# Performance work log

Hardware: AMD Instinct MI355X
Metric: run time of the kernel (lower is better)

The kernel has to match this reference:

```python
import jax, jax.numpy as jnp
import numpy as np

N = 100000          # active sites
C_IN = 256          # inplanes == outplanes
C_MID = 64          # innerplanes
K = 9               # 3x3 kernel offsets (2D)


def setup_inputs() -> dict:
    key = jax.random.key(0)
    ks = jax.random.split(key, 12)
    features = jax.random.normal(ks[0], (N, C_IN), dtype=jnp.float32)
    # submanifold rulebook: for each active site, index of active neighbor per
    # kernel offset; sentinel N = no active neighbor, center (offset 4) = self
    idx = jax.random.randint(ks[1], (N, K), 0, N, dtype=jnp.int32)
    drop = jax.random.uniform(ks[2], (N, K)) < 0.3
    idx = jnp.where(drop, jnp.int32(N), idx)
    neighbor_idx = idx.at[:, 4].set(jnp.arange(N, dtype=jnp.int32))
    s = 0.05
    return {
        "features": features,
        "neighbor_idx": neighbor_idx,
        "w1": jax.random.normal(ks[3], (C_IN, C_MID), dtype=jnp.float32) * s,
        "scale1": jnp.ones((C_MID,), jnp.float32),
        "bias1": jnp.zeros((C_MID,), jnp.float32),
        "w2": jax.random.normal(ks[4], (K, C_MID, C_MID), dtype=jnp.float32) * s,
        "scale2": jnp.ones((C_MID,), jnp.float32),
        "bias2": jnp.zeros((C_MID,), jnp.float32),
        "w3": jax.random.normal(ks[5], (C_MID, C_IN), dtype=jnp.float32) * s,
        "scale3": jnp.ones((C_IN,), jnp.float32),
        "bias3": jnp.zeros((C_IN,), jnp.float32),
    }


def reference(features, neighbor_idx, w1, scale1, bias1, w2, scale2, bias2,
              w3, scale3, bias3):
    # conv1: 1x1 submanifold conv == per-site matmul; affine BN; ReLU
    out = jax.nn.relu(features @ w1 * scale1 + bias1)            # [N, C_MID]
    # conv2: 3x3 submanifold conv via rulebook gather-matmul-accumulate
    padded = jnp.concatenate([out, jnp.zeros((1, C_MID), out.dtype)], axis=0)
    gathered = padded[neighbor_idx]                               # [N, K, C_MID]
    out = jnp.einsum('nkc,kcd->nd', gathered, w2)                 # [N, C_MID]
    out = jax.nn.relu(out * scale2 + bias2)
    # conv3: 1x1 conv; affine BN; residual add (downsample=None); ReLU
    out = out @ w3 * scale3 + bias3 + features                    # [N, C_IN]
    return jax.nn.relu(out)
```

## Files before the change

### kernel.cpp

```cpp
#include <hip/hip_runtime.h>
#include <stdint.h>

#define C_IN 256
#define C_MID 64
#define KOFF 9

typedef __attribute__((ext_vector_type(8))) short bf16x8;
typedef __attribute__((ext_vector_type(4))) short short4v;
typedef __attribute__((ext_vector_type(4))) float f32x4;
typedef __attribute__((ext_vector_type(4))) float float4v;

__device__ inline unsigned short f2bf(float f) {
    union { float f; unsigned u; } x; x.f = f;
    unsigned r = x.u + 0x7FFFu + ((x.u >> 16) & 1u);
    return (unsigned short)(r >> 16);
}

__global__ void prep_kernel(const float* __restrict__ w1, const float* __restrict__ s1,
                            const float* __restrict__ w2, const float* __restrict__ s2,
                            const float* __restrict__ w3, const float* __restrict__ s3,
                            unsigned short* __restrict__ w1t,
                            unsigned short* __restrict__ w2t,
                            unsigned short* __restrict__ w3t,
                            unsigned short* __restrict__ zrow) {
    int tid = blockIdx.x * blockDim.x + threadIdx.x;
    int stride = gridDim.x * blockDim.x;
    for (int i = tid; i < C_MID * C_IN; i += stride) {
        int n = i / C_IN, k = i % C_IN;
        w1t[i] = f2bf(w1[k * C_MID + n] * s1[n]);
    }
    for (int i = tid; i < KOFF * C_MID * C_MID; i += stride) {
        int k = i / (C_MID * C_MID);
        int r = i % (C_MID * C_MID);
        int d = r / C_MID, c = r % C_MID;
        w2t[i] = f2bf(w2[(k * C_MID + c) * C_MID + d] * s2[d]);
    }
    for (int i = tid; i < C_IN * C_MID; i += stride) {
        int e = i / C_MID, c = i % C_MID;
        w3t[i] = f2bf(w3[c * C_IN + e] * s3[e]);
    }
    for (int i = tid; i < C_MID; i += stride) zrow[i] = 0;
}

__global__ __launch_bounds__(256, 4) void conv1_kernel(
    const float* __restrict__ feat, const unsigned short* __restrict__ w1t,
    const float* __restrict__ b1, unsigned short* __restrict__ out1,
    int N, int ntiles)
{
    __shared__ __align__(16) unsigned short sW1[16384];

    int t = threadIdx.x;
    int wave = t >> 6;
    int lane = t & 63;
    int l15 = lane & 15;
    int quad = lane >> 4;

    const bf16x8* w1c = reinterpret_cast<const bf16x8*>(w1t);
    bf16x8* sW1c = reinterpret_cast<bf16x8*>(sW1);
#pragma unroll
    for (int it = 0; it < 8; ++it) {
        int s = it * 256 + t;
        int l = s & 15, ct = (s >> 4) & 3, q = (s >> 6) & 3, kk = s >> 8;
        sW1c[s] = w1c[(ct * 16 + l) * 32 + kk * 4 + q];
    }
    __syncthreads();

    for (int tile = blockIdx.x; tile < ntiles; tile += gridDim.x) {
        int site = tile * 64 + wave * 16 + l15;
        int sitec = site < N ? site : (N - 1);

        float4v fr0[8];
#pragma unroll
        for (int kk = 0; kk < 4; ++kk) {
            const float4v* p = reinterpret_cast<const float4v*>(
                feat + (size_t)sitec * C_IN + kk * 32 + quad * 8);
            fr0[kk * 2] = p[0];
            fr0[kk * 2 + 1] = p[1];
        }
        __builtin_amdgcn_sched_barrier(0);

        float4v fr1[8];
#pragma unroll
        for (int kk = 0; kk < 4; ++kk) {
            const float4v* p = reinterpret_cast<const float4v*>(
                feat + (size_t)sitec * C_IN + (kk + 4) * 32 + quad * 8);
            fr1[kk * 2] = p[0];
            fr1[kk * 2 + 1] = p[1];
        }
        __builtin_amdgcn_sched_barrier(0);

        f32x4 acc[4] = {};
#pragma unroll
        for (int kk = 0; kk < 4; ++kk) {
            union { unsigned short s[8]; bf16x8 v; } ua;
#pragma unroll
            for (int j = 0; j < 4; ++j) {
                ua.s[j] = f2bf(fr0[kk * 2][j]);
                ua.s[4 + j] = f2bf(fr0[kk * 2 + 1][j]);
            }
#pragma unroll
            for (int ct = 0; ct < 4; ++ct) {
                bf16x8 fa = sW1c[((kk * 4 + quad) * 4 + ct) * 16 + l15];
                acc[ct] = __builtin_amdgcn_mfma_f32_16x16x32_bf16(fa, ua.v, acc[ct], 0, 0, 0);
            }
        }
#pragma unroll
        for (int kk = 0; kk < 4; ++kk) {
            union { unsigned short s[8]; bf16x8 v; } ua;
#pragma unroll
            for (int j = 0; j < 4; ++j) {
                ua.s[j] = f2bf(fr1[kk * 2][j]);
                ua.s[4 + j] = f2bf(fr1[kk * 2 + 1][j]);
            }
#pragma unroll
            for (int ct = 0; ct < 4; ++ct) {
                bf16x8 fa = sW1c[(((kk + 4) * 4 + quad) * 4 + ct) * 16 + l15];
                acc[ct] = __builtin_amdgcn_mfma_f32_16x16x32_bf16(fa, ua.v, acc[ct], 0, 0, 0);
            }
        }
        if (site < N) {
#pragma unroll
            for (int ct = 0; ct < 4; ++ct) {
                float4v bb = *reinterpret_cast<const float4v*>(b1 + ct * 16 + quad * 4);
                union { unsigned short s[4]; short4v v; } o;
#pragma unroll
                for (int reg = 0; reg < 4; ++reg)
                    o.s[reg] = f2bf(fmaxf(acc[ct][reg] + bb[reg], 0.f));
                *reinterpret_cast<short4v*>(out1 + (size_t)site * C_MID + ct * 16 + quad * 4) = o.v;
            }
        }
    }
}

__global__ __launch_bounds__(256, 2) void conv23_kernel(
    const float* __restrict__ feat, const int* __restrict__ nbr,
    const unsigned short* __restrict__ out1, const unsigned short* __restrict__ w2t,
    const float* __restrict__ b2, const unsigned short* __restrict__ w3t,
    const float* __restrict__ b3, float* __restrict__ out, int N)
{
    __shared__ __align__(16) unsigned short sWB[21504];
    __shared__ int sNbr[64 * KOFF];

    int t = threadIdx.x;
    int wave = t >> 6;
    int lane = t & 63;
    int l15 = lane & 15;
    int quad = lane >> 4;
    int rt = wave * 16 + l15;
    int site = blockIdx.x * 64 + rt;
    int sitec = site < N ? site : (N - 1);

    bf16x8* sWBc = reinterpret_cast<bf16x8*>(sWB);
    const bf16x8* w2c = reinterpret_cast<const bf16x8*>(w2t);

#pragma unroll
    for (int it = 0; it < 10; ++it) {
        int s = it * 256 + t;
        int l = s & 15, ct = (s >> 4) & 3, q = (s >> 6) & 3, kk = (s >> 8) & 1, k = s >> 9;
        sWBc[s] = w2c[k * 512 + (ct * 16 + l) * 8 + kk * 4 + q];
    }
#pragma unroll
    for (int i = 0; i < 3; ++i) {
        int j = i * 256 + t;
        if (j < 64 * KOFF) {
            int g = blockIdx.x * 64 * KOFF + j;
            sNbr[j] = (g < N * KOFF) ? nbr[g] : N;
        }
    }
    __syncthreads();

    int nb[KOFF];
#pragma unroll
    for (int k = 0; k < KOFF; ++k) nb[k] = sNbr[rt * KOFF + k];

    bf16x8 ga[KOFF][2];
#pragma unroll
    for (int k = 0; k < KOFF; ++k) {
        const bf16x8* pg = reinterpret_cast<const bf16x8*>(out1 + (size_t)nb[k] * C_MID + quad * 8);
        ga[k][0] = pg[0];
        ga[k][1] = pg[4];
    }
    __builtin_amdgcn_sched_barrier(0);

    f32x4 acc2[4] = {};
#pragma unroll
    for (int k = 0; k < 5; ++k) {
#pragma unroll
        for (int kk = 0; kk < 2; ++kk) {
#pragma unroll
            for (int ct = 0; ct < 4; ++ct) {
                bf16x8 fa = sWBc[((k * 2 + kk) * 4 + quad) * 64 + ct * 16 + l15];
                acc2[ct] = __builtin_amdgcn_mfma_f32_16x16x32_bf16(fa, ga[k][kk], acc2[ct], 0, 0, 0);
            }
        }
    }
    __syncthreads();

#pragma unroll
    for (int it = 0; it < 8; ++it) {
        int s = it * 256 + t;
        int l = s & 15, ct = (s >> 4) & 3, q = (s >> 6) & 3, kk = (s >> 8) & 1, k2 = s >> 9;
        sWBc[s] = w2c[(5 + k2) * 512 + (ct * 16 + l) * 8 + kk * 4 + q];
    }
    __syncthreads();
#pragma unroll
    for (int k = 5; k < KOFF; ++k) {
        int kloc = k - 5;
#pragma unroll
        for (int kk = 0; kk < 2; ++kk) {
#pragma unroll
            for (int ct = 0; ct < 4; ++ct) {
                bf16x8 fa = sWBc[((kloc * 2 + kk) * 4 + quad) * 64 + ct * 16 + l15];
                acc2[ct] = __builtin_amdgcn_mfma_f32_16x16x32_bf16(fa, ga[k][kk], acc2[ct], 0, 0, 0);
            }
        }
    }
    float4v rf[16];
#pragma unroll
    for (int c2 = 0; c2 < 16; ++c2)
        rf[c2] = __builtin_nontemporal_load(reinterpret_cast<const float4v*>(
            feat + (size_t)sitec * C_IN + c2 * 16 + quad * 4));
    __builtin_amdgcn_sched_barrier(0);
    __syncthreads();

    unsigned short* mid = &sWB[16384];
#pragma unroll
    for (int ct = 0; ct < 4; ++ct) {
        float4v bb = *reinterpret_cast<const float4v*>(b2 + ct * 16 + quad * 4);
        union { unsigned short s[4]; short4v v; } o;
#pragma unroll
        for (int reg = 0; reg < 4; ++reg)
            o.s[reg] = f2bf(fmaxf(acc2[ct][reg] + bb[reg], 0.f));
        *reinterpret_cast<short4v*>(&mid[rt * 72 + ct * 16 + quad * 4]) = o.v;
    }
    const bf16x8* w3c = reinterpret_cast<const bf16x8*>(w3t);
#pragma unroll
    for (int it = 0; it < 8; ++it) {
        int s = it * 256 + t;
        int l = s & 15, c2 = (s >> 4) & 15, q = (s >> 8) & 3, kk = (s >> 10) & 1;
        sWBc[s] = w3c[(c2 * 16 + l) * 8 + kk * 4 + q];
    }
    __syncthreads();

    f32x4 acc3[16] = {};
#pragma unroll
    for (int kk = 0; kk < 2; ++kk) {
        bf16x8 fb = *reinterpret_cast<const bf16x8*>(
            &mid[rt * 72 + kk * 32 + quad * 8]);
#pragma unroll
        for (int c2 = 0; c2 < 16; ++c2) {
            bf16x8 fa = sWBc[((kk * 4 + quad) * 16 + c2) * 16 + l15];
            acc3[c2] = __builtin_amdgcn_mfma_f32_16x16x32_bf16(fa, fb, acc3[c2], 0, 0, 0);
        }
    }
    if (site < N) {
#pragma unroll
        for (int c2 = 0; c2 < 16; ++c2) {
            float4v bb = *reinterpret_cast<const float4v*>(b3 + c2 * 16 + quad * 4);
            float4v o;
#pragma unroll
            for (int reg = 0; reg < 4; ++reg)
                o[reg] = fmaxf(acc3[c2][reg] + bb[reg] + rf[c2][reg], 0.f);
            __builtin_nontemporal_store(o, reinterpret_cast<float4v*>(
                out + (size_t)site * C_IN + c2 * 16 + quad * 4));
        }
    }
}

extern "C" void kernel_launch(void* const* d_in, const int* in_sizes, int n_in,
                              void* d_out, int out_size, void* d_ws, size_t ws_size,
                              hipStream_t stream) {
    const float* feat = (const float*)d_in[0];
    const int*   nbr  = (const int*)d_in[1];
    const float* w1   = (const float*)d_in[2];
    const float* s1   = (const float*)d_in[3];
    const float* b1   = (const float*)d_in[4];
    const float* w2   = (const float*)d_in[5];
    const float* s2   = (const float*)d_in[6];
    const float* b2   = (const float*)d_in[7];
    const float* w3   = (const float*)d_in[8];
    const float* s3   = (const float*)d_in[9];
    const float* b3   = (const float*)d_in[10];
    float* out = (float*)d_out;
    int N = in_sizes[0] / C_IN;

    char* ws = (char*)d_ws;
    unsigned short* w1t  = (unsigned short*)(ws);
    unsigned short* w2t  = (unsigned short*)(ws + 32768);
    unsigned short* w3t  = (unsigned short*)(ws + 32768 + 73728);
    unsigned short* out1 = (unsigned short*)(ws + 139264);

    prep_kernel<<<80, 256, 0, stream>>>(w1, s1, w2, s2, w3, s3, w1t, w2t, w3t,
                                        out1 + (size_t)N * C_MID);
    int ntiles = (N + 63) / 64;
    int nblk1 = ntiles < 1024 ? ntiles : 1024;
    conv1_kernel<<<nblk1, 256, 0, stream>>>(feat, w1t, b1, out1, N, ntiles);
    conv23_kernel<<<ntiles, 256, 0, stream>>>(feat, nbr, out1, w2t, b2, w3t, b3, out, N);
}
```

Before: 259.2 us.

## Make conv23 persistent with all weights resident in LDS and prefetched neighbors

```diff
diff --git a/kernel.cpp b/kernel.cpp
--- a/kernel.cpp
+++ b/kernel.cpp
@@ -132,14 +132,14 @@
     }
 }
 
-__global__ __launch_bounds__(256, 2) void conv23_kernel(
+__global__ __launch_bounds__(512, 2) void conv23_kernel(
     const float* __restrict__ feat, const int* __restrict__ nbr,
     const unsigned short* __restrict__ out1, const unsigned short* __restrict__ w2t,
     const float* __restrict__ b2, const unsigned short* __restrict__ w3t,
-    const float* __restrict__ b3, float* __restrict__ out, int N)
+    const float* __restrict__ b3, float* __restrict__ out, int N, int ntiles)
 {
-    __shared__ __align__(16) unsigned short sWB[21504];
-    __shared__ int sNbr[64 * KOFF];
+    __shared__ __align__(16) unsigned short sW[53248];
+    __shared__ __align__(16) unsigned short sMid[128 * 72];
 
     int t = threadIdx.x;
     int wave = t >> 6;
@@ -147,123 +147,120 @@
     int l15 = lane & 15;
     int quad = lane >> 4;
     int rt = wave * 16 + l15;
-    int site = blockIdx.x * 64 + rt;
-    int sitec = site < N ? site : (N - 1);
-
-    bf16x8* sWBc = reinterpret_cast<bf16x8*>(sWB);
+
+    bf16x8* sWc = reinterpret_cast<bf16x8*>(sW);
     const bf16x8* w2c = reinterpret_cast<const bf16x8*>(w2t);
-
-#pragma unroll
-    for (int it = 0; it < 10; ++it) {
-        int s = it * 256 + t;
+    const bf16x8* w3c = reinterpret_cast<const bf16x8*>(w3t);
+
+#pragma unroll
+    for (int it = 0; it < 9; ++it) {
+        int s = it * 512 + t;
         int l = s & 15, ct = (s >> 4) & 3, q = (s >> 6) & 3, kk = (s >> 8) & 1, k = s >> 9;
-        sWBc[s] = w2c[k * 512 + (ct * 16 + l) * 8 + kk * 4 + q];
-    }
-#pragma unroll
-    for (int i = 0; i < 3; ++i) {
-        int j = i * 256 + t;
-        if (j < 64 * KOFF) {
-            int g = blockIdx.x * 64 * KOFF + j;
-            sNbr[j] = (g < N * KOFF) ? nbr[g] : N;
-        }
+        sWc[s] = w2c[k * 512 + (ct * 16 + l) * 8 + kk * 4 + q];
+    }
+#pragma unroll
+    for (int it = 0; it < 4; ++it) {
+        int s = it * 512 + t;
+        int l = s & 15, c2 = (s >> 4) & 15, q = (s >> 8) & 3, kk = (s >> 10) & 1;
+        sWc[4608 + s] = w3c[(c2 * 16 + l) * 8 + kk * 4 + q];
     }
     __syncthreads();
 
     int nb[KOFF];
-#pragma unroll
-    for (int k = 0; k < KOFF; ++k) nb[k] = sNbr[rt * KOFF + k];
-
-    bf16x8 ga[KOFF][2];
-#pragma unroll
-    for (int k = 0; k < KOFF; ++k) {
-        const bf16x8* pg = reinterpret_cast<const bf16x8*>(out1 + (size_t)nb[k] * C_MID + quad * 8);
-        ga[k][0] = pg[0];
-        ga[k][1] = pg[4];
-    }
-    __builtin_amdgcn_sched_barrier(0);
-
-    f32x4 acc2[4] = {};
-#pragma unroll
-    for (int k = 0; k < 5; ++k) {
+    {
+        int site0 = blockIdx.x * 128 + rt;
+        bool v0 = site0 < N;
+        int base0 = v0 ? site0 * KOFF : 0;
+#pragma unroll
+        for (int k = 0; k < KOFF; ++k) {
+            int tmp = nbr[base0 + k];
+            nb[k] = v0 ? tmp : N;
+        }
+    }
+
+    for (int tile = blockIdx.x; tile < ntiles; tile += gridDim.x) {
+        int site = tile * 128 + rt;
+        int sitec = site < N ? site : (N - 1);
+
+        bf16x8 ga[KOFF][2];
+#pragma unroll
+        for (int k = 0; k < KOFF; ++k) {
+            const bf16x8* pg = reinterpret_cast<const bf16x8*>(
+                out1 + (size_t)nb[k] * C_MID + quad * 8);
+            ga[k][0] = pg[0];
+            ga[k][1] = pg[4];
+        }
+        __builtin_amdgcn_sched_barrier(0);
+
+        int nnb[KOFF];
+        {
+            int ntile = tile + gridDim.x;
+            int nsite = ntile * 128 + rt;
+            bool v = (ntile < ntiles) && (nsite < N);
+            int nbase = v ? nsite * KOFF : 0;
+#pragma unroll
+            for (int k = 0; k < KOFF; ++k) {
+                int tmp = nbr[nbase + k];
+                nnb[k] = v ? tmp : N;
+            }
+        }
+        __builtin_amdgcn_sched_barrier(0);
+
+        f32x4 acc2[4] = {};
+#pragma unroll
+        for (int k = 0; k < KOFF; ++k) {
+#pragma unroll
+            for (int kk = 0; kk < 2; ++kk) {
+#pragma unroll
+                for (int ct = 0; ct < 4; ++ct) {
+                    bf16x8 fa = sWc[((k * 2 + kk) * 4 + quad) * 64 + ct * 16 + l15];
+                    acc2[ct] = __builtin_amdgcn_mfma_f32_16x16x32_bf16(fa, ga[k][kk], acc2[ct], 0, 0, 0);
+                }
+            }
+        }
+
+#pragma unroll
+        for (int ct = 0; ct < 4; ++ct) {
+            float4v bb = *reinterpret_cast<const float4v*>(b2 + ct * 16 + quad * 4);
+            union { unsigned short s[4]; short4v v; } o;
+#pragma unroll
+            for (int reg = 0; reg < 4; ++reg)
+                o.s[reg] = f2bf(fmaxf(acc2[ct][reg] + bb[reg], 0.f));
+            *reinterpret_cast<short4v*>(&sMid[rt * 72 + ct * 16 + quad * 4]) = o.v;
+        }
+
+        float4v rf[16];
+#pragma unroll
+        for (int c2 = 0; c2 < 16; ++c2)
+            rf[c2] = __builtin_nontemporal_load(reinterpret_cast<const float4v*>(
+                feat + (size_t)sitec * C_IN + c2 * 16 + quad * 4));
+        __builtin_amdgcn_sched_barrier(0);
+
+        f32x4 acc3[16] = {};
 #pragma unroll
         for (int kk = 0; kk < 2; ++kk) {
-#pragma unroll
-            for (int ct = 0; ct < 4; ++ct) {
-                bf16x8 fa = sWBc[((k * 2 + kk) * 4 + quad) * 64 + ct * 16 + l15];
-                acc2[ct] = __builtin_amdgcn_mfma_f32_16x16x32_bf16(fa, ga[k][kk], acc2[ct], 0, 0, 0);
-            }
-        }
-    }
-    __syncthreads();
-
-#pragma unroll
-    for (int it = 0; it < 8; ++it) {
-        int s = it * 256 + t;
-        int l = s & 15, ct = (s >> 4) & 3, q = (s >> 6) & 3, kk = (s >> 8) & 1, k2 = s >> 9;
-        sWBc[s] = w2c[(5 + k2) * 512 + (ct * 16 + l) * 8 + kk * 4 + q];
-    }
-    __syncthreads();
-#pragma unroll
-    for (int k = 5; k < KOFF; ++k) {
-        int kloc = k - 5;
-#pragma unroll
-        for (int kk = 0; kk < 2; ++kk) {
-#pragma unroll
-            for (int ct = 0; ct < 4; ++ct) {
-                bf16x8 fa = sWBc[((kloc * 2 + kk) * 4 + quad) * 64 + ct * 16 + l15];
-                acc2[ct] = __builtin_amdgcn_mfma_f32_16x16x32_bf16(fa, ga[k][kk], acc2[ct], 0, 0, 0);
-            }
-        }
-    }
-    float4v rf[16];
-#pragma unroll
-    for (int c2 = 0; c2 < 16; ++c2)
-        rf[c2] = __builtin_nontemporal_load(reinterpret_cast<const float4v*>(
-            feat + (size_t)sitec * C_IN + c2 * 16 + quad * 4));
-    __builtin_amdgcn_sched_barrier(0);
-    __syncthreads();
-
-    unsigned short* mid = &sWB[16384];
-#pragma unroll
-    for (int ct = 0; ct < 4; ++ct) {
-        float4v bb = *reinterpret_cast<const float4v*>(b2 + ct * 16 + quad * 4);
-        union { unsigned short s[4]; short4v v; } o;
-#pragma unroll
-        for (int reg = 0; reg < 4; ++reg)
-            o.s[reg] = f2bf(fmaxf(acc2[ct][reg] + bb[reg], 0.f));
-        *reinterpret_cast<short4v*>(&mid[rt * 72 + ct * 16 + quad * 4]) = o.v;
-    }
-    const bf16x8* w3c = reinterpret_cast<const bf16x8*>(w3t);
-#pragma unroll
-    for (int it = 0; it < 8; ++it) {
-        int s = it * 256 + t;
-        int l = s & 15, c2 = (s >> 4) & 15, q = (s >> 8) & 3, kk = (s >> 10) & 1;
-        sWBc[s] = w3c[(c2 * 16 + l) * 8 + kk * 4 + q];
-    }
-    __syncthreads();
-
-    f32x4 acc3[16] = {};
-#pragma unroll
-    for (int kk = 0; kk < 2; ++kk) {
-        bf16x8 fb = *reinterpret_cast<const bf16x8*>(
-            &mid[rt * 72 + kk * 32 + quad * 8]);
-#pragma unroll
-        for (int c2 = 0; c2 < 16; ++c2) {
-            bf16x8 fa = sWBc[((kk * 4 + quad) * 16 + c2) * 16 + l15];
-            acc3[c2] = __builtin_amdgcn_mfma_f32_16x16x32_bf16(fa, fb, acc3[c2], 0, 0, 0);
-        }
-    }
-    if (site < N) {
-#pragma unroll
-        for (int c2 = 0; c2 < 16; ++c2) {
-            float4v bb = *reinterpret_cast<const float4v*>(b3 + c2 * 16 + quad * 4);
-            float4v o;
-#pragma unroll
-            for (int reg = 0; reg < 4; ++reg)
-                o[reg] = fmaxf(acc3[c2][reg] + bb[reg] + rf[c2][reg], 0.f);
-            __builtin_nontemporal_store(o, reinterpret_cast<float4v*>(
-                out + (size_t)site * C_IN + c2 * 16 + quad * 4));
-        }
+            bf16x8 fb = *reinterpret_cast<const bf16x8*>(
+                &sMid[rt * 72 + kk * 32 + quad * 8]);
+#pragma unroll
+            for (int c2 = 0; c2 < 16; ++c2) {
+                bf16x8 fa = sWc[4608 + ((kk * 4 + quad) * 16 + c2) * 16 + l15];
+                acc3[c2] = __builtin_amdgcn_mfma_f32_16x16x32_bf16(fa, fb, acc3[c2], 0, 0, 0);
+            }
+        }
+        if (site < N) {
+#pragma unroll
+            for (int c2 = 0; c2 < 16; ++c2) {
+                float4v bb = *reinterpret_cast<const float4v*>(b3 + c2 * 16 + quad * 4);
+                float4v o;
+#pragma unroll
+                for (int reg = 0; reg < 4; ++reg)
+                    o[reg] = fmaxf(acc3[c2][reg] + bb[reg] + rf[c2][reg], 0.f);
+                __builtin_nontemporal_store(o, reinterpret_cast<float4v*>(
+                    out + (size_t)site * C_IN + c2 * 16 + quad * 4));
+            }
+        }
+#pragma unroll
+        for (int k = 0; k < KOFF; ++k) nb[k] = nnb[k];
     }
 }
 
@@ -292,8 +289,11 @@
 
     prep_kernel<<<80, 256, 0, stream>>>(w1, s1, w2, s2, w3, s3, w1t, w2t, w3t,
                                         out1 + (size_t)N * C_MID);
-    int ntiles = (N + 63) / 64;
-    int nblk1 = ntiles < 1024 ? ntiles : 1024;
-    conv1_kernel<<<nblk1, 256, 0, stream>>>(feat, w1t, b1, out1, N, ntiles);
-    conv23_kernel<<<ntiles, 256, 0, stream>>>(feat, nbr, out1, w2t, b2, w3t, b3, out, N);
-}
+    int ntiles1 = (N + 63) / 64;
+    int nblk1 = ntiles1 < 1024 ? ntiles1 : 1024;
+    conv1_kernel<<<nblk1, 256, 0, stream>>>(feat, w1t, b1, out1, N, ntiles1);
+    int ntiles23 = (N + 127) / 128;
+    int nblk23 = ntiles23 < 256 ? ntiles23 : 256;
+    conv23_kernel<<<nblk23, 512, 0, stream>>>(feat, nbr, out1, w2t, b2, w3t, b3, out,
+                                              N, ntiles23);
+}
```

New measurement: 260.0 us. About the same (+0.3%).
